# Performance work log

Measured on AMD Instinct MI355X. Metric: run time of the kernel, lower is better.

Reference implementation:

```python
import jax, jax.numpy as jnp
import numpy as np

# StyleGAN3 constants
FILTER_SIZE = 6
LRELU_UPSAMPLE = 2
SAMPLING_RATE = 128
CUTOFF = 64
HALF_WIDTH = 32
SLOPE = 0.01

UP = LRELU_UPSAMPLE                       # tmp_resize_factor = 2
NUM_TAPS = FILTER_SIZE * UP               # 12
_pad_total = -1 + (NUM_TAPS - 1) * 2      # 21
PAD_LO = (_pad_total + UP) // 2           # 11
PAD_HI = _pad_total - PAD_LO              # 10


def design_lowpass_filter(numtaps, cutoff, width, fs):
    """numpy re-implementation of scipy.signal.firwin(numtaps, cutoff, width=width, fs=fs)."""
    nyq = 0.5 * fs
    # kaiser_atten / kaiser_beta (scipy formulas)
    wn = width / nyq
    a = 2.285 * (numtaps - 1) * np.pi * wn + 7.95
    if a > 50:
        beta = 0.1102 * (a - 8.7)
    elif a > 21:
        beta = 0.5842 * (a - 21) ** 0.4 + 0.07886 * (a - 21)
    else:
        beta = 0.0
    alpha = 0.5 * (numtaps - 1)
    m = np.arange(numtaps) - alpha
    c = cutoff / nyq
    h = c * np.sinc(c * m) * np.kaiser(numtaps, beta)
    h = h / h.sum()  # scale so DC gain == 1 (firwin scale=True for lowpass)
    return jnp.asarray(h, dtype=jnp.float32)


def setup_inputs() -> dict:
    key = jax.random.key(0)
    x = jax.random.normal(key, (8, 128, 128, 128), dtype=jnp.float32)
    f = design_lowpass_filter(NUM_TAPS, CUTOFF, HALF_WIDTH * 2, SAMPLING_RATE * UP)
    return {"x": x, "f": f}


def _filtered_lrelu(x, f):
    """upfirdn2d(up=2, pad, gain=4) -> leaky_relu (gain=1) -> upfirdn2d(down=2)."""
    N, C, H, W = x.shape
    xr = x.reshape(N * C, 1, H, W)            # depthwise via batch folding
    fk = f[::-1].astype(x.dtype)              # conv (not xcorr), matches torch upfirdn2d flip
    dn = ("NCHW", "OIHW", "NCHW")
    g = jnp.asarray(UP, x.dtype)              # up**2 total gain, split over the 2 separable passes
    # --- upsample by 2 (zero insertion via lhs_dilation) + separable FIR ---
    # lhs_dilation yields length 2H-1 (no trailing zero) -> fold the trailing zero into pad_hi (+up-1)
    kv = (fk * g).reshape(1, 1, -1, 1)
    y = jax.lax.conv_general_dilated(xr, kv, (1, 1), ((PAD_LO, PAD_HI + UP - 1), (0, 0)),
                                     lhs_dilation=(UP, UP), dimension_numbers=dn)
    kh = (fk * g).reshape(1, 1, 1, -1)
    y = jax.lax.conv_general_dilated(y, kh, (1, 1), ((0, 0), (PAD_LO, PAD_HI + UP - 1)),
                                     dimension_numbers=dn)
    # --- leaky ReLU (overall gain = 1.0, clamp = None) ---
    y = jnp.where(y >= 0, y, y * jnp.asarray(SLOPE, y.dtype))
    # --- separable FIR + downsample by 2 (stride) ---
    y = jax.lax.conv_general_dilated(y, fk.reshape(1, 1, -1, 1), (UP, 1), ((0, 0), (0, 0)),
                                     dimension_numbers=dn)
    y = jax.lax.conv_general_dilated(y, fk.reshape(1, 1, 1, -1), (1, UP), ((0, 0), (0, 0)),
                                     dimension_numbers=dn)
    Ho, Wo = y.shape[-2], y.shape[-1]         # == H, W
    return y.reshape(N, C, Ho, Wo)


def reference(x, f):
    return _filtered_lrelu(x, f)
```

## Files before the change

kernel.cpp:

```cpp
#include <hip/hip_runtime.h>


#define TAPS 12
#define VS2 0
#define VSS2 44
#define ZS 1628
#define ZSS 44
#define XS2 1628
#define XSS2 26
#define WS 0
#define WSS 44
#define LDS_DW 4884

typedef _Float16 half_t;
typedef half_t h2 __attribute__((ext_vector_type(2)));
typedef __fp16 g2 __attribute__((ext_vector_type(2)));

__device__ __forceinline__ h2 u2h(unsigned u){ h2 r; __builtin_memcpy(&r, &u, 4); return r; }
__device__ __forceinline__ g2 u2g(unsigned u){ g2 r; __builtin_memcpy(&r, &u, 4); return r; }
__device__ __forceinline__ unsigned h2du(h2 h){ unsigned u; __builtin_memcpy(&u, &h, 4); return u; }
__device__ __forceinline__ unsigned pkrtz_u(float lo, float hi){
    g2 p = __builtin_amdgcn_cvt_pkrtz(lo, hi);
    unsigned u; __builtin_memcpy(&u, &p, 4); return u;
}
__device__ __forceinline__ h2 h2s(float v){ h2 r; r.x = (half_t)v; r.y = r.x; return r; }
__device__ __forceinline__ unsigned pack2(half_t a, half_t b){ h2 t; t.x=a; t.y=b; return h2du(t); }

__global__ __launch_bounds__(256) void flrelu_fused(
    const float* __restrict__ x, const float* __restrict__ f, float* __restrict__ out)
{
    __shared__ float smem[LDS_DW];
    unsigned* smemu = reinterpret_cast<unsigned*>(smem);

    const int tid = threadIdx.x;
    const int nc  = blockIdx.y;
    const int ho0 = (blockIdx.x >> 2) * 32;
    const int wo0 = (blockIdx.x & 3) * 32;

    float fkU[TAPS];
#pragma unroll
    for (int t = 0; t < TAPS; ++t) fkU[t] = 2.0f * f[TAPS - 1 - t];

    const float* xin = x + (size_t)nc * (128 * 128);

    if (tid < 242) {
        int p = tid % 22, r0 = tid / 22;
        int ic = wo0 - 6 + 2 * p;
        bool colok = (unsigned)ic < 128u;
        int icc = ic < 0 ? 0 : (ic > 126 ? 126 : ic);
#pragma unroll
        for (int k = 0; k < 4; ++k) {
            int r = r0 + 11 * k;
            if (r < 42) {
                int gr = ho0 - 5 + r;
                int grc = gr < 0 ? 0 : (gr > 127 ? 127 : gr);
                float2 v = *(const float2*)(xin + grc * 128 + icc);
                unsigned pk = pkrtz_u(v.x, v.y);
                bool ok = colok && ((unsigned)gr < 128u);
                smemu[XS2 + r * XSS2 + p] = ok ? pk : 0u;
            }
        }
    }
    __syncthreads();

    if (tid < 209) {
        int g = tid % 11, mc = tid / 11;
        h2 xa[7], xb[7];
#pragma unroll
        for (int s = 0; s < 7; ++s) {
            int r = 2 * mc + s; r = r < 42 ? r : 41;
            uint2 u = *(const uint2*)(smemu + XS2 + r * XSS2 + 2 * g);
            xa[s] = u2h(u.x); xb[s] = u2h(u.y);
        }
        h2 fo[6], fe[6];
#pragma unroll
        for (int s = 0; s < 6; ++s) { fo[s] = h2s(fkU[2*s+1]); fe[s] = h2s(fkU[2*s]); }
#pragma unroll
        for (int k2 = 0; k2 < 2; ++k2) {
            int m = 2 * mc + k2;
            if (m < 37) {
                h2 ea = h2s(0.f), eb = h2s(0.f), oa = h2s(0.f), ob = h2s(0.f);
#pragma unroll
                for (int s = 0; s < 6; ++s) {
                    ea += fo[s] * xa[k2 + s];  eb += fo[s] * xb[k2 + s];
                    oa += fe[s] * xa[k2 + s];  ob += fe[s] * xb[k2 + s];
                }
                unsigned* vp = smemu + VS2 + m * VSS2 + 4 * g;
                *(uint4*)vp = make_uint4(pack2(ea.x, oa.x), pack2(ea.y, oa.y),
                                         pack2(eb.x, ob.x), pack2(eb.y, ob.y));
            }
        }
    }
    __syncthreads();

    if (tid < 185) {
        int q = tid % 5, m = tid / 5;
        const unsigned* vb = smemu + VS2 + m * VSS2 + 8 * q;
        uint4 rr0 = *(const uint4*)(vb);
        uint4 rr1 = *(const uint4*)(vb + 4);
        uint4 rr2 = *(const uint4*)(vb + 8);
        uint2 rr3 = *(const uint2*)(vb + 12);
        h2 vc[13] = { u2h(rr0.y), u2h(rr0.z), u2h(rr0.w),
                      u2h(rr1.x), u2h(rr1.y), u2h(rr1.z), u2h(rr1.w),
                      u2h(rr2.x), u2h(rr2.y), u2h(rr2.z), u2h(rr2.w),
                      u2h(rr3.x), u2h(rr3.y) };
        h2 fo[6], fe[6];
#pragma unroll
        for (int s = 0; s < 6; ++s) { fo[s] = h2s(fkU[2*s+1]); fe[s] = h2s(fkU[2*s]); }
        h2 sl = h2s(0.01f);
        unsigned pk0[8], pk1[8];
#pragma unroll
        for (int h = 0; h < 8; ++h) {
            h2 ae = h2s(0.f), ao = h2s(0.f);
#pragma unroll
            for (int s = 0; s < 6; ++s) {
                ae += vc[h + s] * fo[s];
                ao += vc[h + s] * fe[s];
            }
            ae = __builtin_elementwise_max(ae, ae * sl);
            ao = __builtin_elementwise_max(ao, ao * sl);
            pk0[h] = pack2(ae.x, ao.x);
            pk1[h] = pack2(ae.y, ao.y);
        }
        unsigned* z0 = smemu + ZS + (2 * m) * ZSS + 8 * q;
        unsigned* z1 = z0 + ZSS;
        *(uint4*)(z0)     = make_uint4(pk0[0], pk0[1], pk0[2], pk0[3]);
        *(uint4*)(z0 + 4) = make_uint4(pk0[4], pk0[5], pk0[6], pk0[7]);
        *(uint4*)(z1)     = make_uint4(pk1[0], pk1[1], pk1[2], pk1[3]);
        *(uint4*)(z1 + 4) = make_uint4(pk1[4], pk1[5], pk1[6], pk1[7]);
    }
    __syncthreads();

    if (tid < 80) {
        int p8 = tid % 10, hq = tid / 10;
        h2 fkh[TAPS];
#pragma unroll
        for (int t = 0; t < TAPS; ++t) fkh[t] = h2s(0.5f * fkU[t]);
        h2 acc[4][4];
#pragma unroll
        for (int j = 0; j < 4; ++j)
#pragma unroll
            for (int d = 0; d < 4; ++d) acc[j][d] = h2s(0.f);
        const unsigned* zbase = smemu + ZS + (8 * hq) * ZSS + 4 * p8;
#pragma unroll
        for (int u = 0; u < 18; ++u) {
            uint4 zr = *(const uint4*)(zbase + u * ZSS);
            h2 z0 = u2h(zr.x), z1 = u2h(zr.y), z2 = u2h(zr.z), z3 = u2h(zr.w);
#pragma unroll
            for (int j = 0; j < 4; ++j) {
                int t = u - 2 * j;
                if (t >= 0 && t < TAPS) {
                    h2 tt = fkh[t];
                    acc[j][0] += tt * z0; acc[j][1] += tt * z1;
                    acc[j][2] += tt * z2; acc[j][3] += tt * z3;
                }
            }
        }
        unsigned* wp = smemu + WS + (4 * hq) * WSS + 4 * p8;
#pragma unroll
        for (int j = 0; j < 4; ++j)
            *(uint4*)(wp + j * WSS) = make_uint4(h2du(acc[j][0]), h2du(acc[j][1]),
                                                 h2du(acc[j][2]), h2du(acc[j][3]));
    }
    __syncthreads();

    {
        int ho = tid >> 3, w4 = tid & 7;
        const unsigned* wp = smemu + WS + ho * WSS + 4 * w4;
        uint4 q0 = *(const uint4*)(wp);
        uint4 q1 = *(const uint4*)(wp + 4);
        unsigned q2 = wp[8];
        unsigned dws[9] = { q0.x, q0.y, q0.z, q0.w, q1.x, q1.y, q1.z, q1.w, q2 };
        unsigned fp[6];
#pragma unroll
        for (int d = 0; d < 6; ++d) fp[d] = pkrtz_u(0.5f * fkU[2*d], 0.5f * fkU[2*d+1]);
        float o[4];
#pragma unroll
        for (int v = 0; v < 4; ++v) {
            float acc = 0.f;
#pragma unroll
            for (int d = 0; d < 6; ++d)
                acc = __builtin_amdgcn_fdot2(u2g(dws[v + d]), u2g(fp[d]), acc, false);
            o[v] = acc;
        }
        *(float4*)(out + ((size_t)nc * 128 + (ho0 + ho)) * 128 + wo0 + 4 * w4)
            = make_float4(o[0], o[1], o[2], o[3]);
    }
}

extern "C" void kernel_launch(void* const* d_in, const int* in_sizes, int n_in,
                              void* d_out, int out_size, void* d_ws, size_t ws_size,
                              hipStream_t stream) {
    const float* x = (const float*)d_in[0];
    const float* f = (const float*)d_in[1];
    float* out = (float*)d_out;
    dim3 grid(16, 1024);
    flrelu_fused<<<grid, 256, 0, stream>>>(x, f, out);
}
```

Before: 62.21 us.

## Pack input row-pairs in LDS and use fdot2 for the vertical upsample pass

Input staging now stores each pair of vertically adjacent input rows as packed halves per column, so one 32-bit word holds two rows. Staging uses 441 tasks, each loading a 2x2 input patch, instead of the earlier float2 row loads. The vertical upsample FIR then runs as fdot2 with fp32 accumulation over those row pairs, replacing packed-half FMAs with half accumulation. The goal is fewer VALU ops in the first filter stage; in exchange, global loads become scalar and less coalesced, and the column window offset shifts, which the horizontal stage absorbs by reading one more element.

```diff
diff --git a/kernel.cpp b/kernel.cpp
--- a/kernel.cpp
+++ b/kernel.cpp
@@ -6,8 +6,8 @@
 #define VSS2 44
 #define ZS 1628
 #define ZSS 44
-#define XS2 1628
-#define XSS2 26
+#define XP 1628
+#define XPS 44
 #define WS 0
 #define WSS 44
 #define LDS_DW 4884
@@ -43,52 +43,82 @@
 
     const float* xin = x + (size_t)nc * (128 * 128);
 
-    if (tid < 242) {
-        int p = tid % 22, r0 = tid / 22;
-        int ic = wo0 - 6 + 2 * p;
-        bool colok = (unsigned)ic < 128u;
-        int icc = ic < 0 ? 0 : (ic > 126 ? 126 : ic);
-#pragma unroll
-        for (int k = 0; k < 4; ++k) {
-            int r = r0 + 11 * k;
-            if (r < 42) {
-                int gr = ho0 - 5 + r;
-                int grc = gr < 0 ? 0 : (gr > 127 ? 127 : gr);
-                float2 v = *(const float2*)(xin + grc * 128 + icc);
-                unsigned pk = pkrtz_u(v.x, v.y);
-                bool ok = colok && ((unsigned)gr < 128u);
-                smemu[XS2 + r * XSS2 + p] = ok ? pk : 0u;
-            }
+#pragma unroll
+    for (int it = 0; it < 2; ++it) {
+        int task = tid + 256 * it;
+        if (task < 441) {
+            int c2 = task % 21, p = task / 21;
+            int ic0 = wo0 - 5 + 2 * c2, ic1 = ic0 + 1;
+            int g0 = ho0 - 5 + 2 * p, g1 = g0 + 1;
+            int g0c = g0 < 0 ? 0 : (g0 > 127 ? 127 : g0);
+            int g1c = g1 < 0 ? 0 : (g1 > 127 ? 127 : g1);
+            int ic0c = ic0 < 0 ? 0 : (ic0 > 127 ? 127 : ic0);
+            int ic1c = ic1 < 0 ? 0 : (ic1 > 127 ? 127 : ic1);
+            const float* r0p = xin + g0c * 128;
+            const float* r1p = xin + g1c * 128;
+            float x00 = r0p[ic0c], x01 = r0p[ic1c];
+            float x10 = r1p[ic0c], x11 = r1p[ic1c];
+            bool r0ok = (unsigned)g0 < 128u, r1ok = (unsigned)g1 < 128u;
+            bool c0ok = (unsigned)ic0 < 128u, c1ok = (unsigned)ic1 < 128u;
+            x00 = (r0ok && c0ok) ? x00 : 0.f;
+            x10 = (r1ok && c0ok) ? x10 : 0.f;
+            x01 = (r0ok && c1ok) ? x01 : 0.f;
+            x11 = (r1ok && c1ok) ? x11 : 0.f;
+            unsigned d0 = pkrtz_u(x00, x10);
+            unsigned d1 = pkrtz_u(x01, x11);
+            *(uint2*)(smemu + XP + p * XPS + 2 * c2) = make_uint2(d0, d1);
         }
     }
     __syncthreads();
 
     if (tid < 209) {
-        int g = tid % 11, mc = tid / 11;
-        h2 xa[7], xb[7];
-#pragma unroll
-        for (int s = 0; s < 7; ++s) {
-            int r = 2 * mc + s; r = r < 42 ? r : 41;
-            uint2 u = *(const uint2*)(smemu + XS2 + r * XSS2 + 2 * g);
-            xa[s] = u2h(u.x); xb[s] = u2h(u.y);
-        }
-        h2 fo[6], fe[6];
-#pragma unroll
-        for (int s = 0; s < 6; ++s) { fo[s] = h2s(fkU[2*s+1]); fe[s] = h2s(fkU[2*s]); }
-#pragma unroll
-        for (int k2 = 0; k2 < 2; ++k2) {
-            int m = 2 * mc + k2;
-            if (m < 37) {
-                h2 ea = h2s(0.f), eb = h2s(0.f), oa = h2s(0.f), ob = h2s(0.f);
-#pragma unroll
-                for (int s = 0; s < 6; ++s) {
-                    ea += fo[s] * xa[k2 + s];  eb += fo[s] * xb[k2 + s];
-                    oa += fe[s] * xa[k2 + s];  ob += fe[s] * xb[k2 + s];
-                }
-                unsigned* vp = smemu + VS2 + m * VSS2 + 4 * g;
-                *(uint4*)vp = make_uint4(pack2(ea.x, oa.x), pack2(ea.y, oa.y),
-                                         pack2(eb.x, ob.x), pack2(eb.y, ob.y));
-            }
+        int cq = tid % 11, mc = tid / 11;
+        uint4 P[4];
+#pragma unroll
+        for (int i = 0; i < 4; ++i) {
+            int pp = mc + i; pp = pp < 21 ? pp : 20;
+            P[i] = *(const uint4*)(smemu + XP + pp * XPS + 4 * cq);
+        }
+        unsigned a0[4] = { P[0].x, P[0].y, P[0].z, P[0].w };
+        unsigned a1[4] = { P[1].x, P[1].y, P[1].z, P[1].w };
+        unsigned a2[4] = { P[2].x, P[2].y, P[2].z, P[2].w };
+        unsigned a3[4] = { P[3].x, P[3].y, P[3].z, P[3].w };
+        unsigned te0 = pkrtz_u(fkU[1], fkU[3]),  te1 = pkrtz_u(fkU[5], fkU[7]),
+                 te2 = pkrtz_u(fkU[9], fkU[11]), to0 = pkrtz_u(fkU[0], fkU[2]),
+                 to1 = pkrtz_u(fkU[4], fkU[6]),  to2 = pkrtz_u(fkU[8], fkU[10]);
+        unsigned se1 = pkrtz_u(fkU[3], fkU[5]),  se2 = pkrtz_u(fkU[7], fkU[9]),
+                 so1 = pkrtz_u(fkU[2], fkU[4]),  so2 = pkrtz_u(fkU[6], fkU[8]),
+                 ee  = pkrtz_u(fkU[1], fkU[11]), eo  = pkrtz_u(fkU[0], fkU[10]);
+        {
+            unsigned w0[4];
+#pragma unroll
+            for (int j = 0; j < 4; ++j) {
+                float ve = __builtin_amdgcn_fdot2(u2g(a0[j]), u2g(te0), 0.f, false);
+                ve = __builtin_amdgcn_fdot2(u2g(a1[j]), u2g(te1), ve, false);
+                ve = __builtin_amdgcn_fdot2(u2g(a2[j]), u2g(te2), ve, false);
+                float vo = __builtin_amdgcn_fdot2(u2g(a0[j]), u2g(to0), 0.f, false);
+                vo = __builtin_amdgcn_fdot2(u2g(a1[j]), u2g(to1), vo, false);
+                vo = __builtin_amdgcn_fdot2(u2g(a2[j]), u2g(to2), vo, false);
+                w0[j] = pkrtz_u(ve, vo);
+            }
+            *(uint4*)(smemu + VS2 + (2 * mc) * VSS2 + 4 * cq)
+                = make_uint4(w0[0], w0[1], w0[2], w0[3]);
+        }
+        if (2 * mc + 1 < 37) {
+            unsigned w1[4];
+#pragma unroll
+            for (int j = 0; j < 4; ++j) {
+                unsigned edge = pack2(u2h(a0[j]).y, u2h(a3[j]).x);
+                float ve = __builtin_amdgcn_fdot2(u2g(a1[j]), u2g(se1), 0.f, false);
+                ve = __builtin_amdgcn_fdot2(u2g(a2[j]), u2g(se2), ve, false);
+                ve = __builtin_amdgcn_fdot2(u2g(edge),  u2g(ee),  ve, false);
+                float vo = __builtin_amdgcn_fdot2(u2g(a1[j]), u2g(so1), 0.f, false);
+                vo = __builtin_amdgcn_fdot2(u2g(a2[j]), u2g(so2), vo, false);
+                vo = __builtin_amdgcn_fdot2(u2g(edge),  u2g(eo),  vo, false);
+                w1[j] = pkrtz_u(ve, vo);
+            }
+            *(uint4*)(smemu + VS2 + (2 * mc + 1) * VSS2 + 4 * cq)
+                = make_uint4(w1[0], w1[1], w1[2], w1[3]);
         }
     }
     __syncthreads();
@@ -100,7 +130,7 @@
         uint4 rr1 = *(const uint4*)(vb + 4);
         uint4 rr2 = *(const uint4*)(vb + 8);
         uint2 rr3 = *(const uint2*)(vb + 12);
-        h2 vc[13] = { u2h(rr0.y), u2h(rr0.z), u2h(rr0.w),
+        h2 vc[14] = { u2h(rr0.x), u2h(rr0.y), u2h(rr0.z), u2h(rr0.w),
                       u2h(rr1.x), u2h(rr1.y), u2h(rr1.z), u2h(rr1.w),
                       u2h(rr2.x), u2h(rr2.y), u2h(rr2.z), u2h(rr2.w),
                       u2h(rr3.x), u2h(rr3.y) };
```

Result: no change. 62.20 us (-0.0%).
